# Performance work log

Measured on AMD Instinct MI355X. Metric: run time of the kernel, lower is better.

Reference implementation:

```python
import jax, jax.numpy as jnp
import numpy as np

D_MODEL = 1024
D_FF = 4096
N_EXPERTS = 8
TOP_K = 2

def setup_inputs() -> dict:
    key = jax.random.key(0)
    ks = jax.random.split(key, 8)
    s = 0.02
    return {
        "x": jax.random.normal(ks[0], (4, 2048, D_MODEL), dtype=jnp.float32),
        "W1": jax.random.normal(ks[1], (N_EXPERTS, D_MODEL, D_FF), dtype=jnp.float32) * s,
        "b1": jnp.zeros((N_EXPERTS, D_FF), dtype=jnp.float32),
        "W2": jax.random.normal(ks[2], (N_EXPERTS, D_FF, D_MODEL), dtype=jnp.float32) * s,
        "b2": jnp.zeros((N_EXPERTS, D_MODEL), dtype=jnp.float32),
        "Wg": jax.random.normal(ks[3], (D_MODEL, N_EXPERTS), dtype=jnp.float32) * s,
        "bg": jnp.zeros((N_EXPERTS,), dtype=jnp.float32),
    }

def reference(x, W1, b1, W2, b2, Wg, bg):
    B, S, D = x.shape
    # Gating network
    gate_logits = jnp.einsum('bsd,de->bse', x, Wg) + bg
    gate_probs = jax.nn.softmax(gate_logits, axis=-1)  # (B,S,E)
    # Top-k routing on softmax probs (matches torch.topk(F.softmax(logits)))
    top_k_probs, top_k_indices = jax.lax.top_k(gate_probs, TOP_K)  # (B,S,k)
    T = B * S
    x_flat = x.reshape(T, D)
    idx_flat = top_k_indices.reshape(T, TOP_K)
    prob_flat = top_k_probs.reshape(T, TOP_K)
    # Per-token combine weight for each expert: sum of top-k probs routed to it
    # combine[t, e] = sum_j prob_flat[t, j] * (idx_flat[t, j] == e)
    onehot = jax.nn.one_hot(idx_flat, N_EXPERTS, dtype=x.dtype)  # (T,k,E)
    combine = jnp.einsum('tk,tke->te', prob_flat, onehot)  # (T,E)
    out = jnp.zeros((T, D), dtype=x.dtype)
    for e in range(N_EXPERTS):  # static small loop over experts
        h = jax.nn.relu(x_flat @ W1[e] + b1[e])  # (T, d_ff)
        y = h @ W2[e] + b2[e]                    # (T, d_model)
        out = out + combine[:, e:e+1] * y
    return out.reshape(B, S, D), gate_probs
```

## Files before the change

### kernel.cpp

```cpp
#include <hip/hip_runtime.h>

#define D_MODEL 1024
#define D_FF    4096
#define N_EXP   8
#define BM 128
#define BN 128
#define BK 32

typedef __attribute__((ext_vector_type(8))) short bf16x8;
typedef __attribute__((ext_vector_type(4))) float f32x4;
typedef unsigned int u32;

__device__ __forceinline__ unsigned short f2bf(float f) {
  union { float f; unsigned u; } v; v.f = f;
  unsigned r = v.u + 0x7FFFu + ((v.u >> 16) & 1u);
  return (unsigned short)(r >> 16);
}

__device__ __forceinline__ void gl_lds16(const void* g, void* l) {
  __builtin_amdgcn_global_load_lds((const __attribute__((address_space(1))) u32*)g,
                                   (__attribute__((address_space(3))) u32*)l, 16, 0, 0);
}

__global__ __launch_bounds__(256)
void transpose_convert_kernel(const float* __restrict__ src, unsigned short* __restrict__ dst,
                              int Ksub, int Nsrc,
                              unsigned long long eStride) {
  __shared__ u32 s32k[32][65];
  int e = blockIdx.z;
  int kb = blockIdx.x * 64, nb = blockIdx.y * 64;
  const float* se = src + (size_t)e * eStride + (size_t)kb * Nsrc + nb;
  unsigned short* de = dst + (size_t)e * (size_t)Nsrc * Ksub + (size_t)nb * Ksub + kb;
  int tid = threadIdx.x;
  int kh = tid >> 4;
  int n4 = (tid & 15) * 4;
  #pragma unroll
  for (int p = 0; p < 2; p++) {
    int k = kh * 2 + p * 32;
    float4 v0 = *(const float4*)(se + (size_t)k * Nsrc + n4);
    float4 v1 = *(const float4*)(se + (size_t)(k + 1) * Nsrc + n4);
    #pragma unroll
    for (int j = 0; j < 4; j++) {
      u32 pk = (u32)f2bf(((const float*)&v0)[j]) |
               ((u32)f2bf(((const float*)&v1)[j]) << 16);
      s32k[k >> 1][n4 + j] = pk;
    }
  }
  __syncthreads();
  #pragma unroll
  for (int c = 0; c < 2; c++) {
    int id = tid + c * 256;
    int n = id >> 3, kc = id & 7;
    uint4 o;
    o.x = s32k[kc * 4 + 0][n];
    o.y = s32k[kc * 4 + 1][n];
    o.z = s32k[kc * 4 + 2][n];
    o.w = s32k[kc * 4 + 3][n];
    *(uint4*)(de + (size_t)n * Ksub + kc * 8) = o;
  }
}

__global__ void gating_kernel(const float* __restrict__ x,
                              const float* __restrict__ Wg,
                              const float* __restrict__ bg,
                              float* __restrict__ gate_out,
                              unsigned short* __restrict__ xb,
                              int* __restrict__ cnt,
                              int* __restrict__ tokIdx,
                              float* __restrict__ tokW, int T) {
  int wv = threadIdx.x >> 6, lane = threadIdx.x & 63;
  int t = blockIdx.x * 4 + wv;
  if (t >= T) return;
  const float* xr = x + (size_t)t * D_MODEL + lane * 16;
  float acc[N_EXP];
  #pragma unroll
  for (int e = 0; e < N_EXP; e++) acc[e] = 0.f;
  ushort4 xc[4];
  #pragma unroll
  for (int q = 0; q < 4; q++) {
    float4 xv = *(const float4*)(xr + q * 4);
    xc[q].x = f2bf(xv.x); xc[q].y = f2bf(xv.y);
    xc[q].z = f2bf(xv.z); xc[q].w = f2bf(xv.w);
    #pragma unroll
    for (int r = 0; r < 4; r++) {
      float xs = ((const float*)&xv)[r];
      const float* wrow = Wg + (size_t)(lane * 16 + q * 4 + r) * N_EXP;
      float4 wa = *(const float4*)wrow;
      float4 wb = *(const float4*)(wrow + 4);
      acc[0] += xs * wa.x; acc[1] += xs * wa.y; acc[2] += xs * wa.z; acc[3] += xs * wa.w;
      acc[4] += xs * wb.x; acc[5] += xs * wb.y; acc[6] += xs * wb.z; acc[7] += xs * wb.w;
    }
  }
  unsigned short* xbr = xb + (size_t)t * D_MODEL + lane * 16;
  #pragma unroll
  for (int q = 0; q < 4; q++) *(ushort4*)(xbr + q * 4) = xc[q];
  #pragma unroll
  for (int off = 32; off > 0; off >>= 1) {
    #pragma unroll
    for (int e = 0; e < N_EXP; e++) acc[e] += __shfl_xor(acc[e], off);
  }
  if (lane == 0) {
    float l[N_EXP], p[N_EXP];
    float m = -1e30f;
    #pragma unroll
    for (int e = 0; e < N_EXP; e++) { l[e] = acc[e] + bg[e]; m = fmaxf(m, l[e]); }
    float s = 0.f;
    #pragma unroll
    for (int e = 0; e < N_EXP; e++) { p[e] = __expf(l[e] - m); s += p[e]; }
    float inv = 1.f / s;
    #pragma unroll
    for (int e = 0; e < N_EXP; e++) { p[e] *= inv; gate_out[(size_t)t * N_EXP + e] = p[e]; }
    int e1 = 0;
    #pragma unroll
    for (int e = 1; e < N_EXP; e++) if (p[e] > p[e1]) e1 = e;
    int e2 = (e1 == 0) ? 1 : 0;
    #pragma unroll
    for (int e = 0; e < N_EXP; e++) if (e != e1 && p[e] > p[e2]) e2 = e;
    int pos = atomicAdd(cnt + e1, 1);
    tokIdx[(size_t)e1 * T + pos] = t; tokW[(size_t)e1 * T + pos] = p[e1];
    pos = atomicAdd(cnt + e2, 1);
    tokIdx[(size_t)e2 * T + pos] = t; tokW[(size_t)e2 * T + pos] = p[e2];
  }
}

__global__ void schedule_kernel(const int* __restrict__ cnt, int* __restrict__ meta,
                                int* __restrict__ tE, int* __restrict__ tB,
                                int* __restrict__ tV, int T, int maxTiles) {
  if (threadIdx.x != 0 || blockIdx.x != 0) return;
  int t = 0;
  for (int e = 0; e < N_EXP; e++) {
    int c = cnt[e];
    for (int r = 0; r < c && t < maxTiles; r += BM) {
      tE[t] = e; tB[t] = e * T + r; tV[t] = min(BM, c - r); t++;
    }
  }
  meta[0] = t;
}

#define STAGE(b, kt) { _Pragma("unroll") for (int p_ = 0; p_ < 2; p_++) { \
    gl_lds16(srcA[p_] + (size_t)(kt) * BK, &LDSU[(b) * 8192 + (w * 32 + p_ * 16) * 32]); \
    gl_lds16(srcB[p_] + (size_t)(kt) * BK, &LDSU[(b) * 8192 + 4096 + (w * 32 + p_ * 16) * 32]); } }

#define COMPUTE(b) { \
    bf16x8 ra[4], rb[4]; \
    _Pragma("unroll") for (int m_ = 0; m_ < 4; m_++) { \
      int row_ = wr * 64 + m_ * 16 + l15; \
      ra[m_] = *(const bf16x8*)&LDSU[(b) * 8192 + row_ * 32 + (((l4 + (row_ >> 1)) & 3) << 3)]; } \
    _Pragma("unroll") for (int n_ = 0; n_ < 4; n_++) { \
      int rb_ = wc * 64 + n_ * 16 + l15; \
      rb[n_] = *(const bf16x8*)&LDSU[(b) * 8192 + 4096 + rb_ * 32 + (((l4 + (rb_ >> 1)) & 3) << 3)]; } \
    _Pragma("unroll") for (int m_ = 0; m_ < 4; m_++) \
      _Pragma("unroll") for (int n_ = 0; n_ < 4; n_++) \
        acc[m_][n_] = __builtin_amdgcn_mfma_f32_16x16x32_bf16(ra[m_], rb[n_], acc[m_][n_], 0, 0, 0); }

#define BAR() { __builtin_amdgcn_s_barrier(); asm volatile("" ::: "memory"); }
#define WAITVM(N) asm volatile("s_waitcnt vmcnt(" #N ")" ::: "memory");

#define PIPE3(NT) \
  STAGE(0, 0); STAGE(1, 1); \
  for (int it = 0; it < ((NT) - 2) / 3; it++) { \
    int kt = 3 * it; \
    STAGE(2, kt + 2); WAITVM(8); BAR(); COMPUTE(0); BAR(); \
    STAGE(0, kt + 3); WAITVM(8); BAR(); COMPUTE(1); BAR(); \
    STAGE(1, kt + 4); WAITVM(8); BAR(); COMPUTE(2); BAR(); \
  } \
  WAITVM(4); BAR(); COMPUTE(0); BAR(); \
  WAITVM(0); BAR(); COMPUTE(1);

__global__ __launch_bounds__(256)
void gemm1_kernel(const unsigned short* __restrict__ xb,
                  const unsigned short* __restrict__ w1t,
                  const float* __restrict__ b1,
                  const int* __restrict__ meta,
                  const int* __restrict__ tE, const int* __restrict__ tB,
                  const int* __restrict__ tV, const int* __restrict__ tokIdx,
                  unsigned short* __restrict__ h) {
  __shared__ unsigned short LDSU[24576];

  int total = gridDim.x;
  int L = blockIdx.x;
  int q = total >> 3, r8 = total & 7;
  int xcd = L & 7, idx = L >> 3;
  int work = (xcd < r8) ? (xcd * (q + 1) + idx) : (r8 * (q + 1) + (xcd - r8) * q + idx);
  int tile = work >> 5;
  int cb = work & 31;
  if (tile >= meta[0]) return;
  int e = tE[tile], base = tB[tile], valid = tV[tile];
  int tid = threadIdx.x;

  int w = tid >> 6, lane = tid & 63;
  int wr = w >> 1, wc = w & 1;
  int l15 = lane & 15, l4 = lane >> 4;
  int lrow = lane >> 2, lch = lane & 3;

  const unsigned short* panel = w1t + (size_t)e * D_FF * D_MODEL;
  const unsigned short* srcA[2];
  const unsigned short* srcB[2];
  #pragma unroll
  for (int p = 0; p < 2; p++) {
    int r = w * 32 + p * 16 + lrow;
    int tok = tokIdx[base + (r < valid ? r : valid - 1)];
    int g = (lch - (r >> 1)) & 3;
    srcA[p] = xb + (size_t)tok * D_MODEL + g * 8;
    srcB[p] = panel + (size_t)(cb * BN + r) * D_MODEL + g * 8;
  }

  f32x4 acc[4][4];
  #pragma unroll
  for (int m = 0; m < 4; m++)
    #pragma unroll
    for (int n = 0; n < 4; n++) acc[m][n] = (f32x4){0.f, 0.f, 0.f, 0.f};

  PIPE3(D_MODEL / BK);

  #pragma unroll
  for (int n = 0; n < 4; n++) {
    int colc = cb * BN + wc * 64 + n * 16 + l15;
    float bias = b1[(size_t)e * D_FF + colc];
    #pragma unroll
    for (int m = 0; m < 4; m++) {
      #pragma unroll
      for (int r = 0; r < 4; r++) {
        int row = wr * 64 + m * 16 + l4 * 4 + r;
        float v = acc[m][n][r] + bias;
        v = v > 0.f ? v : 0.f;
        h[(size_t)(tile * BM + row) * D_FF + colc] = f2bf(v);
      }
    }
  }
}

__global__ __launch_bounds__(256)
void gemm2_kernel(const unsigned short* __restrict__ h,
                  const unsigned short* __restrict__ w2t,
                  const float* __restrict__ b2,
                  const int* __restrict__ meta,
                  const int* __restrict__ tE, const int* __restrict__ tB,
                  const int* __restrict__ tV, const int* __restrict__ tokIdx,
                  const float* __restrict__ tokW,
                  float* __restrict__ out) {
  __shared__ unsigned short LDSU[24576];

  int total = gridDim.x;
  int L = blockIdx.x;
  int q = total >> 3, r8 = total & 7;
  int xcd = L & 7, idx = L >> 3;
  int work = (xcd < r8) ? (xcd * (q + 1) + idx) : (r8 * (q + 1) + (xcd - r8) * q + idx);
  int tile = work >> 3;
  int cb = work & 7;
  if (tile >= meta[0]) return;
  int e = tE[tile], base = tB[tile], valid = tV[tile];
  int tid = threadIdx.x;

  int w = tid >> 6, lane = tid & 63;
  int wr = w >> 1, wc = w & 1;
  int l15 = lane & 15, l4 = lane >> 4;
  int lrow = lane >> 2, lch = lane & 3;

  const unsigned short* panel = w2t + (size_t)e * D_MODEL * D_FF;
  const unsigned short* srcA[2];
  const unsigned short* srcB[2];
  #pragma unroll
  for (int p = 0; p < 2; p++) {
    int r = w * 32 + p * 16 + lrow;
    int g = (lch - (r >> 1)) & 3;
    srcA[p] = h + (size_t)(tile * BM + r) * D_FF + g * 8;
    srcB[p] = panel + (size_t)(cb * BN + r) * D_FF + g * 8;
  }

  f32x4 acc[4][4];
  #pragma unroll
  for (int m = 0; m < 4; m++)
    #pragma unroll
    for (int n = 0; n < 4; n++) acc[m][n] = (f32x4){0.f, 0.f, 0.f, 0.f};

  PIPE3(D_FF / BK);

  float biasv[4];
  #pragma unroll
  for (int n = 0; n < 4; n++)
    biasv[n] = b2[(size_t)e * D_MODEL + cb * BN + wc * 64 + n * 16 + l15];

  #pragma unroll
  for (int m = 0; m < 4; m++) {
    #pragma unroll
    for (int r = 0; r < 4; r++) {
      int row = wr * 64 + m * 16 + l4 * 4 + r;
      if (row < valid) {
        int tok = tokIdx[base + row];
        float wgt = tokW[base + row];
        float* orow = out + (size_t)tok * D_MODEL + cb * BN + wc * 64 + l15;
        #pragma unroll
        for (int n = 0; n < 4; n++)
          atomicAdd(orow + n * 16, (acc[m][n][r] + biasv[n]) * wgt);
      }
    }
  }
}

extern "C" void kernel_launch(void* const* d_in, const int* in_sizes, int n_in,
                              void* d_out, int out_size, void* d_ws, size_t ws_size,
                              hipStream_t stream) {
  const float* x  = (const float*)d_in[0];
  const float* W1 = (const float*)d_in[1];
  const float* b1 = (const float*)d_in[2];
  const float* W2 = (const float*)d_in[3];
  const float* b2 = (const float*)d_in[4];
  const float* Wg = (const float*)d_in[5];
  const float* bg = (const float*)d_in[6];

  int T = in_sizes[0] / D_MODEL;
  float* out = (float*)d_out;
  float* gate_out = out + (size_t)T * D_MODEL;

  char* ws = (char*)d_ws;
  int* cnt  = (int*)(ws + 0);
  int* meta = (int*)(ws + 64);
  int* tE   = (int*)(ws + 128);
  int* tB   = (int*)(ws + 1024);
  int* tV   = (int*)(ws + 2048);
  size_t off = 4096;
  int* tokIdx = (int*)(ws + off);   off += (size_t)N_EXP * T * 4;
  float* tokW = (float*)(ws + off); off += (size_t)N_EXP * T * 4;
  unsigned short* xb = (unsigned short*)(ws + off); off += (size_t)T * D_MODEL * 2;
  off = (off + 255) & ~(size_t)255;

  int maxTiles = (2 * T) / BM + N_EXP;

  unsigned short* w1t = (unsigned short*)(ws + off); off += (size_t)N_EXP * D_MODEL * D_FF * 2;
  unsigned short* w2t = (unsigned short*)(ws + off); off += (size_t)N_EXP * D_MODEL * D_FF * 2;
  unsigned short* h   = (unsigned short*)(ws + off);

  hipMemsetAsync(d_out, 0, (size_t)T * D_MODEL * sizeof(float), stream);
  hipMemsetAsync(cnt, 0, N_EXP * sizeof(int), stream);

  gating_kernel<<<(T + 3) / 4, 256, 0, stream>>>(x, Wg, bg, gate_out, xb, cnt, tokIdx, tokW, T);
  schedule_kernel<<<1, 64, 0, stream>>>(cnt, meta, tE, tB, tV, T, maxTiles);

  transpose_convert_kernel<<<dim3(D_MODEL / 64, D_FF / 64, N_EXP), 256, 0, stream>>>(
      W1, w1t, D_MODEL, D_FF, (unsigned long long)D_MODEL * D_FF);
  transpose_convert_kernel<<<dim3(D_FF / 64, D_MODEL / 64, N_EXP), 256, 0, stream>>>(
      W2, w2t, D_FF, D_MODEL, (unsigned long long)D_FF * D_MODEL);

  gemm1_kernel<<<maxTiles * (D_FF / BN), 256, 0, stream>>>(
      xb, w1t, b1, meta, tE, tB, tV, tokIdx, h);
  gemm2_kernel<<<maxTiles * (D_MODEL / BN), 256, 0, stream>>>(
      h, w2t, b2, meta, tE, tB, tV, tokIdx, tokW, out);
}
```

Measured before the change: 739.5 us.

## Split-K gemm2, merge weight transposes, reorder gemm1 tile mapping

The second expert GEMM is split four ways along the d_ff reduction. Each slice accumulates into the output with atomics, and only slice 0 adds the bias. This multiplies the number of workgroups, which should fill the GPU better, at the cost of four times more atomic traffic on the output. The two weight transpose/convert launches are merged into a single launch covering both matrices. gemm1's work index is remapped so consecutive blocks walk tiles for the same column block, which changes weight-panel reuse across XCDs.

```diff
diff --git a/kernel.cpp b/kernel.cpp
--- a/kernel.cpp
+++ b/kernel.cpp
@@ -23,14 +23,26 @@
 }
 
 __global__ __launch_bounds__(256)
-void transpose_convert_kernel(const float* __restrict__ src, unsigned short* __restrict__ dst,
-                              int Ksub, int Nsrc,
-                              unsigned long long eStride) {
+void transpose_convert_all(const float* __restrict__ W1, const float* __restrict__ W2,
+                           unsigned short* __restrict__ w1t, unsigned short* __restrict__ w2t) {
   __shared__ u32 s32k[32][65];
-  int e = blockIdx.z;
-  int kb = blockIdx.x * 64, nb = blockIdx.y * 64;
-  const float* se = src + (size_t)e * eStride + (size_t)kb * Nsrc + nb;
-  unsigned short* de = dst + (size_t)e * (size_t)Nsrc * Ksub + (size_t)nb * Ksub + kb;
+  int z = blockIdx.z;
+  const float* se;
+  unsigned short* de;
+  int Ksub, Nsrc, kb, nb;
+  if (z < 8) {
+    Ksub = D_MODEL; Nsrc = D_FF;
+    kb = blockIdx.y * 64; nb = blockIdx.x * 64;
+    se = W1 + (size_t)z * D_MODEL * D_FF;
+    de = w1t + (size_t)z * D_FF * D_MODEL;
+  } else {
+    Ksub = D_FF; Nsrc = D_MODEL;
+    kb = blockIdx.x * 64; nb = blockIdx.y * 64;
+    se = W2 + (size_t)(z - 8) * D_FF * D_MODEL;
+    de = w2t + (size_t)(z - 8) * D_MODEL * D_FF;
+  }
+  se += (size_t)kb * Nsrc + nb;
+  de += (size_t)nb * Ksub + kb;
   int tid = threadIdx.x;
   int kh = tid >> 4;
   int n4 = (tid & 15) * 4;
@@ -174,7 +186,7 @@
                   const int* __restrict__ meta,
                   const int* __restrict__ tE, const int* __restrict__ tB,
                   const int* __restrict__ tV, const int* __restrict__ tokIdx,
-                  unsigned short* __restrict__ h) {
+                  unsigned short* __restrict__ h, int nT) {
   __shared__ unsigned short LDSU[24576];
 
   int total = gridDim.x;
@@ -182,8 +194,8 @@
   int q = total >> 3, r8 = total & 7;
   int xcd = L & 7, idx = L >> 3;
   int work = (xcd < r8) ? (xcd * (q + 1) + idx) : (r8 * (q + 1) + (xcd - r8) * q + idx);
-  int tile = work >> 5;
-  int cb = work & 31;
+  int cb = work / nT;
+  int tile = work - cb * nT;
   if (tile >= meta[0]) return;
   int e = tE[tile], base = tB[tile], valid = tV[tile];
   int tid = threadIdx.x;
@@ -246,7 +258,8 @@
   int q = total >> 3, r8 = total & 7;
   int xcd = L & 7, idx = L >> 3;
   int work = (xcd < r8) ? (xcd * (q + 1) + idx) : (r8 * (q + 1) + (xcd - r8) * q + idx);
-  int tile = work >> 3;
+  int tile = work >> 5;
+  int ks = (work >> 3) & 3;
   int cb = work & 7;
   if (tile >= meta[0]) return;
   int e = tE[tile], base = tB[tile], valid = tV[tile];
@@ -257,6 +270,8 @@
   int l15 = lane & 15, l4 = lane >> 4;
   int lrow = lane >> 2, lch = lane & 3;
 
+  const int ksOff = ks * (D_FF / 4);
+
   const unsigned short* panel = w2t + (size_t)e * D_MODEL * D_FF;
   const unsigned short* srcA[2];
   const unsigned short* srcB[2];
@@ -264,8 +279,8 @@
   for (int p = 0; p < 2; p++) {
     int r = w * 32 + p * 16 + lrow;
     int g = (lch - (r >> 1)) & 3;
-    srcA[p] = h + (size_t)(tile * BM + r) * D_FF + g * 8;
-    srcB[p] = panel + (size_t)(cb * BN + r) * D_FF + g * 8;
+    srcA[p] = h + (size_t)(tile * BM + r) * D_FF + ksOff + g * 8;
+    srcB[p] = panel + (size_t)(cb * BN + r) * D_FF + ksOff + g * 8;
   }
 
   f32x4 acc[4][4];
@@ -274,12 +289,13 @@
     #pragma unroll
     for (int n = 0; n < 4; n++) acc[m][n] = (f32x4){0.f, 0.f, 0.f, 0.f};
 
-  PIPE3(D_FF / BK);
+  PIPE3(D_FF / 4 / BK);
 
   float biasv[4];
+  int addBias = (ks == 0) ? 1 : 0;
   #pragma unroll
   for (int n = 0; n < 4; n++)
-    biasv[n] = b2[(size_t)e * D_MODEL + cb * BN + wc * 64 + n * 16 + l15];
+    biasv[n] = addBias ? b2[(size_t)e * D_MODEL + cb * BN + wc * 64 + n * 16 + l15] : 0.f;
 
   #pragma unroll
   for (int m = 0; m < 4; m++) {
@@ -337,13 +353,10 @@
   gating_kernel<<<(T + 3) / 4, 256, 0, stream>>>(x, Wg, bg, gate_out, xb, cnt, tokIdx, tokW, T);
   schedule_kernel<<<1, 64, 0, stream>>>(cnt, meta, tE, tB, tV, T, maxTiles);
 
-  transpose_convert_kernel<<<dim3(D_MODEL / 64, D_FF / 64, N_EXP), 256, 0, stream>>>(
-      W1, w1t, D_MODEL, D_FF, (unsigned long long)D_MODEL * D_FF);
-  transpose_convert_kernel<<<dim3(D_FF / 64, D_MODEL / 64, N_EXP), 256, 0, stream>>>(
-      W2, w2t, D_FF, D_MODEL, (unsigned long long)D_FF * D_MODEL);
+  transpose_convert_all<<<dim3(64, 16, 16), 256, 0, stream>>>(W1, W2, w1t, w2t);
 
   gemm1_kernel<<<maxTiles * (D_FF / BN), 256, 0, stream>>>(
-      xb, w1t, b1, meta, tE, tB, tV, tokIdx, h);
-  gemm2_kernel<<<maxTiles * (D_MODEL / BN), 256, 0, stream>>>(
+      xb, w1t, b1, meta, tE, tB, tV, tokIdx, h, maxTiles);
+  gemm2_kernel<<<maxTiles * (D_MODEL / BN) * 4, 256, 0, stream>>>(
       h, w2t, b2, meta, tE, tB, tV, tokIdx, tokW, out);
 }
```

Measured after the change: 831.3 us. +12.4%, slower.
